# Performance work log

Hardware: AMD Instinct MI355X
Metric: run time of the kernel (lower is better)

## Reference

```python
import jax, jax.numpy as jnp
import numpy as np

B, F, R, C = 16384, 256, 32, 16
H1, H2 = 128, 32        # FS-MLP hidden sizes
G1, G2 = 256, 64        # consequent MLP hidden sizes


def setup_inputs() -> dict:
    key = jax.random.key(0)
    ks = jax.random.split(key, 16)
    s = 0.05
    return {
        "data": jax.random.normal(ks[0], (B, F), jnp.float32),
        # per-rule antecedent params (torch inits proto=0, var=1; randomize proto for a nontrivial test)
        "proto": jax.random.normal(ks[1], (R, F), jnp.float32) * 0.1,
        "var": jnp.full((R, F), 0.05, jnp.float32),
        # shared FS-MLP: Linear(F,128)->ReLU->Linear(128,32)->ReLU->Linear(32,1)->ReLU
        "Wf1": jax.random.normal(ks[2], (H1, F), jnp.float32) * s,
        "bf1": jax.random.normal(ks[3], (H1,), jnp.float32) * s,
        "Wf2": jax.random.normal(ks[4], (H2, H1), jnp.float32) * s,
        "bf2": jax.random.normal(ks[5], (H2,), jnp.float32) * s,
        "Wf3": jax.random.normal(ks[6], (1, H2), jnp.float32) * s,
        "bf3": jax.random.normal(ks[7], (1,), jnp.float32) * s,
        # per-rule consequent MLP (stacked over rule dim): Linear(F,256)->ELU->Linear(256,64)->ELU->Linear(64,C)
        "Wc1": jax.random.normal(ks[8], (R, G1, F), jnp.float32) * s,
        "bc1": jax.random.normal(ks[9], (R, G1), jnp.float32) * s,
        "Wc2": jax.random.normal(ks[10], (R, G2, G1), jnp.float32) * s,
        "bc2": jax.random.normal(ks[11], (R, G2), jnp.float32) * s,
        "Wc3": jax.random.normal(ks[12], (R, C, G2), jnp.float32) * s,
        "bc3": jax.random.normal(ks[13], (R, C), jnp.float32) * s,
    }


def reference(data, proto, var, Wf1, bf1, Wf2, bf2, Wf3, bf3,
              Wc1, bc1, Wc2, bc2, Wc3, bc3):
    # Antecedent: Gaussian membership per rule -> [R, B, F]
    v = jnp.clip(var, 1e-4, 0.1)
    mem = jnp.exp(-(data[None, :, :] - proto[:, None, :]) ** 2
                  / (2.0 * v[:, None, :] ** 2))
    # Shared firing-strength MLP on each rule's membership tensor -> [R, B]
    h = jax.nn.relu(jnp.einsum('rbf,of->rbo', mem, Wf1) + bf1)
    h = jax.nn.relu(jnp.einsum('rbo,po->rbp', h, Wf2) + bf2)
    fs_ini = jax.nn.relu(jnp.einsum('rbp,qp->rbq', h, Wf3) + bf3)[..., 0]
    fire_strength = jax.nn.softmax(fs_ini.T, axis=1)  # [B, R], softmax over rules
    # Per-rule consequent MLPs on raw data (batched over rule dim) -> [R, B, C]
    c = jax.nn.elu(jnp.einsum('bf,rhf->rbh', data, Wc1) + bc1[:, None, :])
    c = jax.nn.elu(jnp.einsum('rbh,rgh->rbg', c, Wc2) + bc2[:, None, :])
    c = jax.nn.relu(jnp.einsum('rbg,rcg->rbc', c, Wc3) + bc3[:, None, :])
    # Softmax-weighted sum over rules -> [B, C]
    outputs = jnp.einsum('rbc,br->bc', c, fire_strength)
    return outputs, fire_strength
```

## Files before the change

kernel.cpp:

```cpp
#include <hip/hip_runtime.h>
#include <hip/hip_bf16.h>

#define BN 16384
#define FN 256
#define RN 32
#define CN 16
#define H1N 128
#define H2N 32
#define G1N 256
#define G2N 64

typedef __bf16 bf16_t;
typedef __bf16 bf16x8 __attribute__((ext_vector_type(8)));
typedef __bf16 bf16x4 __attribute__((ext_vector_type(4)));
typedef float f32x4 __attribute__((ext_vector_type(4)));

#define OFF_DATA   0UL
#define OFF_WF1    8388608UL
#define OFF_WF2    8454144UL
#define OFF_WC1    8462336UL
#define OFF_WC2    12656640UL
#define OFF_WC3    13705216UL
#define OFF_FSINI  13770752UL
#define OFF_C3     15867904UL

__device__ __forceinline__ f32x4 mfma16(bf16x8 a, bf16x8 b, f32x4 c) {
  return __builtin_amdgcn_mfma_f32_16x16x32_bf16(a, b, c, 0, 0, 0);
}

__device__ __forceinline__ float elu_f(float v) {
  float e = __builtin_amdgcn_exp2f(v * 1.44269504f) - 1.0f;
  return v > 0.f ? v : e;
}

__device__ __forceinline__ bf16x8 lfrag(const char* base, int strideB, int n0, int k0, int lane) {
  int row = n0 + (lane & 15);
  int off = (k0 * 2 + ((lane >> 4) << 4)) ^ ((row & 7) << 4);
  return *(const bf16x8*)(base + row * strideB + off);
}

__device__ __forceinline__ void pack_frag8(const float* __restrict__ src, bf16_t* __restrict__ dst,
                                           int NT, int KS, int g) {
  int per = NT * KS * 64;
  int r = g / per;
  int local = g - r * per;
  int lane = local & 63;
  int fr = local >> 6;
  int ks = fr / NT;
  int nt = fr - ks * NT;
  int N = NT * 16, K = KS * 32;
  int n = nt * 16 + (lane & 15);
  int k = ks * 32 + ((lane >> 4) << 3);
  const float* s = src + (long)r * N * K + (long)n * K + k;
  float4 a = *(const float4*)s;
  float4 b = *(const float4*)(s + 4);
  bf16x8 o;
  o[0] = (bf16_t)a.x; o[1] = (bf16_t)a.y; o[2] = (bf16_t)a.z; o[3] = (bf16_t)a.w;
  o[4] = (bf16_t)b.x; o[5] = (bf16_t)b.y; o[6] = (bf16_t)b.z; o[7] = (bf16_t)b.w;
  *(bf16x8*)(dst + (long)g * 8) = o;
}

#define G_DATA 524288
#define G_WC1  262144
#define G_WC2  65536
#define G_WF1  4096
#define G_WC3  4096
#define G_WF2  512
#define G_TOTAL (G_DATA + G_WC1 + G_WC2 + G_WF1 + G_WC3 + G_WF2)

__global__ __launch_bounds__(256) void k0_pack(
    const float* __restrict__ data, const float* __restrict__ Wf1, const float* __restrict__ Wf2,
    const float* __restrict__ Wc1, const float* __restrict__ Wc2, const float* __restrict__ Wc3,
    char* __restrict__ ws)
{
  int g = blockIdx.x * 256 + threadIdx.x;
  if (g < G_DATA) {
    const float* s = data + (long)g * 8;
    float4 a = *(const float4*)s, b = *(const float4*)(s + 4);
    bf16x8 o;
    o[0] = (bf16_t)a.x; o[1] = (bf16_t)a.y; o[2] = (bf16_t)a.z; o[3] = (bf16_t)a.w;
    o[4] = (bf16_t)b.x; o[5] = (bf16_t)b.y; o[6] = (bf16_t)b.z; o[7] = (bf16_t)b.w;
    *(bf16x8*)((bf16_t*)(ws + OFF_DATA) + (long)g * 8) = o;
    return;
  }
  g -= G_DATA;
  if (g < G_WC1) { pack_frag8(Wc1, (bf16_t*)(ws + OFF_WC1), 16, 8, g); return; }
  g -= G_WC1;
  if (g < G_WC2) { pack_frag8(Wc2, (bf16_t*)(ws + OFF_WC2), 4, 8, g); return; }
  g -= G_WC2;
  if (g < G_WF1) { pack_frag8(Wf1, (bf16_t*)(ws + OFF_WF1), 8, 8, g); return; }
  g -= G_WF1;
  if (g < G_WC3) { pack_frag8(Wc3, (bf16_t*)(ws + OFF_WC3), 1, 2, g); return; }
  g -= G_WC3;
  if (g < G_WF2) { pack_frag8(Wf2, (bf16_t*)(ws + OFF_WF2), 2, 4, g); return; }
}

__global__ __launch_bounds__(512) void k1_fs(
    const float* __restrict__ data, const float* __restrict__ proto, const float* __restrict__ var,
    const float* __restrict__ bf1g, const float* __restrict__ bf2g,
    const float* __restrict__ Wf3g, const float* __restrict__ bf3g,
    const bf16_t* __restrict__ Wf1p, const bf16_t* __restrict__ Wf2p,
    float* __restrict__ fsini)
{
  __shared__ float proto_s[FN];
  __shared__ float ivar_s[FN];
  __shared__ __attribute__((aligned(16))) char fs_lds[36864];

  const int r   = blockIdx.x >> 8;
  const int b0  = (blockIdx.x & 255) << 6;
  const int tid = threadIdx.x;
  const int lane = tid & 63;
  const int w   = tid >> 6;

  if (tid < FN) {
    proto_s[tid] = proto[r * FN + tid];
    float v = var[r * FN + tid];
    v = fminf(fmaxf(v, 1e-4f), 0.1f);
    ivar_s[tid] = 1.4426950408889634f * 0.5f / (v * v);
  }
  __syncthreads();

  {
    const int row = tid >> 3;
    const int f0  = (tid & 7) << 5;
    const float* dp = data + (long)(b0 + row) * FN + f0;
    char* mrow = fs_lds + row * 512;
    const int sw = (row & 7) << 4;
    #pragma unroll
    for (int i = 0; i < 4; ++i) {
      const int f = f0 + i * 8;
      float4 x0 = *(const float4*)(dp + i * 8);
      float4 x1 = *(const float4*)(dp + i * 8 + 4);
      bf16x8 m; float d;
      d = x0.x - proto_s[f + 0]; m[0] = (bf16_t)__builtin_amdgcn_exp2f(-d * d * ivar_s[f + 0]);
      d = x0.y - proto_s[f + 1]; m[1] = (bf16_t)__builtin_amdgcn_exp2f(-d * d * ivar_s[f + 1]);
      d = x0.z - proto_s[f + 2]; m[2] = (bf16_t)__builtin_amdgcn_exp2f(-d * d * ivar_s[f + 2]);
      d = x0.w - proto_s[f + 3]; m[3] = (bf16_t)__builtin_amdgcn_exp2f(-d * d * ivar_s[f + 3]);
      d = x1.x - proto_s[f + 4]; m[4] = (bf16_t)__builtin_amdgcn_exp2f(-d * d * ivar_s[f + 4]);
      d = x1.y - proto_s[f + 5]; m[5] = (bf16_t)__builtin_amdgcn_exp2f(-d * d * ivar_s[f + 5]);
      d = x1.z - proto_s[f + 6]; m[6] = (bf16_t)__builtin_amdgcn_exp2f(-d * d * ivar_s[f + 6]);
      d = x1.w - proto_s[f + 7]; m[7] = (bf16_t)__builtin_amdgcn_exp2f(-d * d * ivar_s[f + 7]);
      *(bf16x8*)(mrow + ((f * 2) ^ sw)) = m;
    }
  }
  __syncthreads();

  const int mg = w >> 1;
  const int ng = w & 1;
  f32x4 acc[2][2] = {};
  #pragma unroll
  for (int ks = 0; ks < 8; ++ks) {
    bf16x8 a[2], bb[2];
    #pragma unroll
    for (int i = 0; i < 2; ++i)
      a[i] = *(const bf16x8*)(Wf1p + (((ks * 8 + mg * 2 + i) * 64 + lane)) * 8);
    #pragma unroll
    for (int j = 0; j < 2; ++j)
      bb[j] = lfrag(fs_lds, 512, (ng * 2 + j) * 16, ks * 32, lane);
    #pragma unroll
    for (int i = 0; i < 2; ++i)
      #pragma unroll
      for (int j = 0; j < 2; ++j)
        acc[i][j] = mfma16(a[i], bb[j], acc[i][j]);
  }
  __syncthreads();

  #pragma unroll
  for (int i = 0; i < 2; ++i) {
    const int hb = (mg * 2 + i) * 16 + ((lane >> 4) << 2);
    f32x4 bias = *(const f32x4*)(bf1g + hb);
    #pragma unroll
    for (int j = 0; j < 2; ++j) {
      const int b = (ng * 2 + j) * 16 + (lane & 15);
      bf16x4 o;
      #pragma unroll
      for (int q = 0; q < 4; ++q)
        o[q] = (bf16_t)fmaxf(acc[i][j][q] + bias[q], 0.f);
      *(bf16x4*)(fs_lds + b * 256 + ((hb * 2) ^ ((b & 7) << 4))) = o;
    }
  }
  __syncthreads();

  bf16_t* h2t = (bf16_t*)(fs_lds + 32768);
  {
    const int m = w >> 2;
    const int n = w & 3;
    f32x4 acc2 = {};
    #pragma unroll
    for (int ks = 0; ks < 4; ++ks) {
      bf16x8 a = *(const bf16x8*)(Wf2p + (((ks * 2 + m) * 64 + lane)) * 8);
      bf16x8 bb = lfrag(fs_lds, 256, n * 16, ks * 32, lane);
      acc2 = mfma16(a, bb, acc2);
    }
    const int p0 = m * 16 + ((lane >> 4) << 2);
    const int b  = n * 16 + (lane & 15);
    f32x4 bias = *(const f32x4*)(bf2g + p0);
    #pragma unroll
    for (int q = 0; q < 4; ++q)
      h2t[(p0 + q) * 64 + b] = (bf16_t)fmaxf(acc2[q] + bias[q], 0.f);
  }
  __syncthreads();

  if (tid < 64) {
    float s = bf3g[0];
    #pragma unroll
    for (int p = 0; p < H2N; ++p) s += (float)h2t[p * 64 + tid] * Wf3g[p];
    fsini[(long)(b0 + tid) * RN + r] = fmaxf(s, 0.f);
  }
}

__global__ __launch_bounds__(256) void k2_softmax(const float* __restrict__ fsini,
                                                  float* __restrict__ fire)
{
  int b = blockIdx.x * 256 + threadIdx.x;
  float v[RN];
  const float4* p = (const float4*)(fsini + (long)b * RN);
  #pragma unroll
  for (int i = 0; i < RN / 4; ++i) {
    float4 t = p[i];
    v[4 * i] = t.x; v[4 * i + 1] = t.y; v[4 * i + 2] = t.z; v[4 * i + 3] = t.w;
  }
  float m = v[0];
  #pragma unroll
  for (int i = 1; i < RN; ++i) m = fmaxf(m, v[i]);
  float s = 0.f;
  #pragma unroll
  for (int i = 0; i < RN; ++i) { v[i] = expf(v[i] - m); s += v[i]; }
  float inv = 1.f / s;
  float4* o = (float4*)(fire + (long)b * RN);
  #pragma unroll
  for (int i = 0; i < RN / 4; ++i) {
    float4 t; t.x = v[4 * i] * inv; t.y = v[4 * i + 1] * inv;
    t.z = v[4 * i + 2] * inv; t.w = v[4 * i + 3] * inv;
    o[i] = t;
  }
}

__global__ __launch_bounds__(512) void k3_cons(
    const bf16_t* __restrict__ datab,
    const bf16_t* __restrict__ Wc1p, const bf16_t* __restrict__ Wc2p, const bf16_t* __restrict__ Wc3p,
    const float* __restrict__ bc1, const float* __restrict__ bc2, const float* __restrict__ bc3,
    float* __restrict__ c3buf)
{
  __shared__ __attribute__((aligned(16))) char a_lds[64 * 512];
  __shared__ __attribute__((aligned(16))) char c2_lds[64 * 128];

  const int bid = blockIdx.x;
  const int xcd = bid & 7;
  const int kk  = bid >> 3;
  const int r   = xcd * 4 + (kk >> 8);
  const int b0  = (kk & 255) << 6;

  const int tid = threadIdx.x;
  const int lane = tid & 63;
  const int w   = tid >> 6;

  {
    const int row = tid >> 3;
    const int e0  = (tid & 7) << 5;
    const bf16_t* sp = datab + (long)(b0 + row) * FN + e0;
    char* drow = a_lds + row * 512;
    const int sw = (row & 7) << 4;
    #pragma unroll
    for (int i = 0; i < 4; ++i) {
      bf16x8 v = *(const bf16x8*)(sp + i * 8);
      *(bf16x8*)(drow + (((e0 + i * 8) * 2) ^ sw)) = v;
    }
  }
  __syncthreads();

  const int wm = w >> 1;
  const int wn = w & 1;
  const bf16_t* W1 = Wc1p + (long)r * G1N * FN;
  f32x4 acc[4][2] = {};
  #pragma unroll
  for (int ks = 0; ks < 8; ++ks) {
    bf16x8 a[4], bb[2];
    #pragma unroll
    for (int i = 0; i < 4; ++i)
      a[i] = *(const bf16x8*)(W1 + (((ks * 16 + wm * 4 + i) * 64 + lane)) * 8);
    #pragma unroll
    for (int j = 0; j < 2; ++j)
      bb[j] = lfrag(a_lds, 512, (wn * 2 + j) * 16, ks * 32, lane);
    #pragma unroll
    for (int i = 0; i < 4; ++i)
      #pragma unroll
      for (int j = 0; j < 2; ++j)
        acc[i][j] = mfma16(a[i], bb[j], acc[i][j]);
  }
  __syncthreads();

  #pragma unroll
  for (int i = 0; i < 4; ++i) {
    const int g1b = (wm * 4 + i) * 16 + ((lane >> 4) << 2);
    f32x4 bias = *(const f32x4*)(bc1 + r * G1N + g1b);
    #pragma unroll
    for (int j = 0; j < 2; ++j) {
      const int b = (wn * 2 + j) * 16 + (lane & 15);
      bf16x4 o;
      #pragma unroll
      for (int q = 0; q < 4; ++q)
        o[q] = (bf16_t)elu_f(acc[i][j][q] + bias[q]);
      *(bf16x4*)(a_lds + b * 512 + ((g1b * 2) ^ ((b & 7) << 4))) = o;
    }
  }
  __syncthreads();

  const int m2 = w >> 1;
  const int n2 = w & 1;
  const bf16_t* W2 = Wc2p + (long)r * G2N * G1N;
  f32x4 acc2[2] = {};
  #pragma unroll
  for (int ks = 0; ks < 8; ++ks) {
    bf16x8 a = *(const bf16x8*)(W2 + (((ks * 4 + m2) * 64 + lane)) * 8);
    #pragma unroll
    for (int j = 0; j < 2; ++j) {
      bf16x8 bb = lfrag(a_lds, 512, (n2 * 2 + j) * 16, ks * 32, lane);
      acc2[j] = mfma16(a, bb, acc2[j]);
    }
  }
  {
    const int g2b = m2 * 16 + ((lane >> 4) << 2);
    f32x4 bias = *(const f32x4*)(bc2 + r * G2N + g2b);
    #pragma unroll
    for (int j = 0; j < 2; ++j) {
      const int b = (n2 * 2 + j) * 16 + (lane & 15);
      bf16x4 o;
      #pragma unroll
      for (int q = 0; q < 4; ++q)
        o[q] = (bf16_t)elu_f(acc2[j][q] + bias[q]);
      *(bf16x4*)(c2_lds + b * 128 + ((g2b * 2) ^ ((b & 7) << 4))) = o;
    }
  }
  __syncthreads();

  if (w < 4) {
    const bf16_t* W3 = Wc3p + (long)r * CN * G2N;
    f32x4 acc3 = {};
    #pragma unroll
    for (int ks = 0; ks < 2; ++ks) {
      bf16x8 a = *(const bf16x8*)(W3 + (((long)ks * 64 + lane)) * 8);
      bf16x8 bb = lfrag(c2_lds, 128, w * 16, ks * 32, lane);
      acc3 = mfma16(a, bb, acc3);
    }
    const int c0 = ((lane >> 4) << 2);
    const int b  = w * 16 + (lane & 15);
    f32x4 bias = *(const f32x4*)(bc3 + r * CN + c0);
    f32x4 o;
    #pragma unroll
    for (int q = 0; q < 4; ++q) o[q] = fmaxf(acc3[q] + bias[q], 0.f);
    *(f32x4*)(c3buf + ((long)r * BN + b0 + b) * CN + c0) = o;
  }
}

__global__ __launch_bounds__(256) void k4_out(const float* __restrict__ c3buf,
                                              const float* __restrict__ fire,
                                              float* __restrict__ out)
{
  int t = blockIdx.x * 256 + threadIdx.x;
  int b = t >> 2, c4 = (t & 3) << 2;
  const float* fp = fire + (long)b * RN;
  f32x4 s = {};
  #pragma unroll
  for (int rr = 0; rr < RN; ++rr) {
    float fw = fp[rr];
    f32x4 v = *(const f32x4*)(c3buf + ((long)rr * BN + b) * CN + c4);
    s += fw * v;
  }
  *(f32x4*)(out + (long)b * CN + c4) = s;
}

extern "C" void kernel_launch(void* const* d_in, const int* in_sizes, int n_in,
                              void* d_out, int out_size, void* d_ws, size_t ws_size,
                              hipStream_t stream) {
  const float* data = (const float*)d_in[0];
  const float* proto = (const float*)d_in[1];
  const float* var  = (const float*)d_in[2];
  const float* Wf1  = (const float*)d_in[3];
  const float* bf1  = (const float*)d_in[4];
  const float* Wf2  = (const float*)d_in[5];
  const float* bf2  = (const float*)d_in[6];
  const float* Wf3  = (const float*)d_in[7];
  const float* bf3  = (const float*)d_in[8];
  const float* Wc1  = (const float*)d_in[9];
  const float* bc1  = (const float*)d_in[10];
  const float* Wc2  = (const float*)d_in[11];
  const float* bc2  = (const float*)d_in[12];
  const float* Wc3  = (const float*)d_in[13];
  const float* bc3  = (const float*)d_in[14];

  char* ws = (char*)d_ws;
  bf16_t* datab = (bf16_t*)(ws + OFF_DATA);
  bf16_t* Wf1p  = (bf16_t*)(ws + OFF_WF1);
  bf16_t* Wf2p  = (bf16_t*)(ws + OFF_WF2);
  bf16_t* Wc1p  = (bf16_t*)(ws + OFF_WC1);
  bf16_t* Wc2p  = (bf16_t*)(ws + OFF_WC2);
  bf16_t* Wc3p  = (bf16_t*)(ws + OFF_WC3);
  float*  fsini = (float*)(ws + OFF_FSINI);
  float*  c3buf = (float*)(ws + OFF_C3);

  float* out  = (float*)d_out;
  float* fire = out + (long)BN * CN;

  k0_pack<<<G_TOTAL / 256, 256, 0, stream>>>(data, Wf1, Wf2, Wc1, Wc2, Wc3, ws);
  k1_fs<<<RN * (BN / 64), 512, 0, stream>>>(data, proto, var, bf1, bf2, Wf3, bf3,
                                            Wf1p, Wf2p, fsini);
  k2_softmax<<<BN / 256, 256, 0, stream>>>(fsini, fire);
  k3_cons<<<RN * (BN / 64), 512, 0, stream>>>(datab, Wc1p, Wc2p, Wc3p, bc1, bc2, bc3, c3buf);
  k4_out<<<(BN * CN / 4) / 256, 256, 0, stream>>>(c3buf, fire, out);
}
```

Baseline: 255.1 us.

## Process four rules per block in firing-strength kernel and raise MFMA wave priority

The firing-strength kernel now handles four rules per block. Each block loads its data tile into registers once and loops over the rules, which cuts the grid from 32×256 to 8×256 blocks and reuses each data row four times instead of re-reading it from global memory. In exchange the kernel holds more registers, runs serial per-rule phases with extra barriers, and has fewer blocks available to hide latency. Separately, the consequent kernel raises wave priority with s_setprio around its MFMA loops so matrix work gets issued ahead of other waves.

```diff
diff --git a/kernel.cpp b/kernel.cpp
--- a/kernel.cpp
+++ b/kernel.cpp
@@ -102,110 +102,127 @@
     const bf16_t* __restrict__ Wf1p, const bf16_t* __restrict__ Wf2p,
     float* __restrict__ fsini)
 {
-  __shared__ float proto_s[FN];
-  __shared__ float ivar_s[FN];
+  __shared__ float proto_s[4][FN];
+  __shared__ float ivar_s[4][FN];
   __shared__ __attribute__((aligned(16))) char fs_lds[36864];
 
-  const int r   = blockIdx.x >> 8;
-  const int b0  = (blockIdx.x & 255) << 6;
+  const int bid = blockIdx.x;
+  const int rg  = bid >> 8;
+  const int b0  = (bid & 255) << 6;
   const int tid = threadIdx.x;
   const int lane = tid & 63;
   const int w   = tid >> 6;
 
-  if (tid < FN) {
-    proto_s[tid] = proto[r * FN + tid];
-    float v = var[r * FN + tid];
+  #pragma unroll
+  for (int k = 0; k < 2; ++k) {
+    int idx = tid + k * 512;
+    int rr = idx >> 8, f = idx & 255;
+    int r = rg * 4 + rr;
+    proto_s[rr][f] = proto[r * FN + f];
+    float v = var[r * FN + f];
     v = fminf(fmaxf(v, 1e-4f), 0.1f);
-    ivar_s[tid] = 1.4426950408889634f * 0.5f / (v * v);
+    ivar_s[rr][f] = 1.4426950408889634f * 0.5f / (v * v);
+  }
+
+  const int row = tid >> 3;
+  const int f0  = (tid & 7) << 5;
+  float4 dreg[8];
+  {
+    const float* dp = data + (long)(b0 + row) * FN + f0;
+    #pragma unroll
+    for (int i = 0; i < 8; ++i) dreg[i] = *(const float4*)(dp + i * 4);
   }
   __syncthreads();
 
-  {
-    const int row = tid >> 3;
-    const int f0  = (tid & 7) << 5;
-    const float* dp = data + (long)(b0 + row) * FN + f0;
-    char* mrow = fs_lds + row * 512;
-    const int sw = (row & 7) << 4;
-    #pragma unroll
-    for (int i = 0; i < 4; ++i) {
-      const int f = f0 + i * 8;
-      float4 x0 = *(const float4*)(dp + i * 8);
-      float4 x1 = *(const float4*)(dp + i * 8 + 4);
-      bf16x8 m; float d;
-      d = x0.x - proto_s[f + 0]; m[0] = (bf16_t)__builtin_amdgcn_exp2f(-d * d * ivar_s[f + 0]);
-      d = x0.y - proto_s[f + 1]; m[1] = (bf16_t)__builtin_amdgcn_exp2f(-d * d * ivar_s[f + 1]);
-      d = x0.z - proto_s[f + 2]; m[2] = (bf16_t)__builtin_amdgcn_exp2f(-d * d * ivar_s[f + 2]);
-      d = x0.w - proto_s[f + 3]; m[3] = (bf16_t)__builtin_amdgcn_exp2f(-d * d * ivar_s[f + 3]);
-      d = x1.x - proto_s[f + 4]; m[4] = (bf16_t)__builtin_amdgcn_exp2f(-d * d * ivar_s[f + 4]);
-      d = x1.y - proto_s[f + 5]; m[5] = (bf16_t)__builtin_amdgcn_exp2f(-d * d * ivar_s[f + 5]);
-      d = x1.z - proto_s[f + 6]; m[6] = (bf16_t)__builtin_amdgcn_exp2f(-d * d * ivar_s[f + 6]);
-      d = x1.w - proto_s[f + 7]; m[7] = (bf16_t)__builtin_amdgcn_exp2f(-d * d * ivar_s[f + 7]);
-      *(bf16x8*)(mrow + ((f * 2) ^ sw)) = m;
-    }
-  }
-  __syncthreads();
-
-  const int mg = w >> 1;
-  const int ng = w & 1;
-  f32x4 acc[2][2] = {};
-  #pragma unroll
-  for (int ks = 0; ks < 8; ++ks) {
-    bf16x8 a[2], bb[2];
-    #pragma unroll
-    for (int i = 0; i < 2; ++i)
-      a[i] = *(const bf16x8*)(Wf1p + (((ks * 8 + mg * 2 + i) * 64 + lane)) * 8);
-    #pragma unroll
-    for (int j = 0; j < 2; ++j)
-      bb[j] = lfrag(fs_lds, 512, (ng * 2 + j) * 16, ks * 32, lane);
-    #pragma unroll
-    for (int i = 0; i < 2; ++i)
+  bf16_t* h2t = (bf16_t*)(fs_lds + 32768);
+  char* mrow = fs_lds + row * 512;
+  const int sw = (row & 7) << 4;
+
+  for (int rr = 0; rr < 4; ++rr) {
+    const int r = rg * 4 + rr;
+
+    {
+      #pragma unroll
+      for (int i = 0; i < 4; ++i) {
+        const int f = f0 + i * 8;
+        float4 x0 = dreg[i * 2];
+        float4 x1 = dreg[i * 2 + 1];
+        bf16x8 m; float d;
+        d = x0.x - proto_s[rr][f + 0]; m[0] = (bf16_t)__builtin_amdgcn_exp2f(-d * d * ivar_s[rr][f + 0]);
+        d = x0.y - proto_s[rr][f + 1]; m[1] = (bf16_t)__builtin_amdgcn_exp2f(-d * d * ivar_s[rr][f + 1]);
+        d = x0.z - proto_s[rr][f + 2]; m[2] = (bf16_t)__builtin_amdgcn_exp2f(-d * d * ivar_s[rr][f + 2]);
+        d = x0.w - proto_s[rr][f + 3]; m[3] = (bf16_t)__builtin_amdgcn_exp2f(-d * d * ivar_s[rr][f + 3]);
+        d = x1.x - proto_s[rr][f + 4]; m[4] = (bf16_t)__builtin_amdgcn_exp2f(-d * d * ivar_s[rr][f + 4]);
+        d = x1.y - proto_s[rr][f + 5]; m[5] = (bf16_t)__builtin_amdgcn_exp2f(-d * d * ivar_s[rr][f + 5]);
+        d = x1.z - proto_s[rr][f + 6]; m[6] = (bf16_t)__builtin_amdgcn_exp2f(-d * d * ivar_s[rr][f + 6]);
+        d = x1.w - proto_s[rr][f + 7]; m[7] = (bf16_t)__builtin_amdgcn_exp2f(-d * d * ivar_s[rr][f + 7]);
+        *(bf16x8*)(mrow + ((f * 2) ^ sw)) = m;
+      }
+    }
+    __syncthreads();
+
+    const int mg = w >> 1;
+    const int ng = w & 1;
+    f32x4 acc[2][2] = {};
+    #pragma unroll
+    for (int ks = 0; ks < 8; ++ks) {
+      bf16x8 a[2], bb[2];
+      #pragma unroll
+      for (int i = 0; i < 2; ++i)
+        a[i] = *(const bf16x8*)(Wf1p + (((ks * 8 + mg * 2 + i) * 64 + lane)) * 8);
       #pragma unroll
       for (int j = 0; j < 2; ++j)
-        acc[i][j] = mfma16(a[i], bb[j], acc[i][j]);
-  }
-  __syncthreads();
-
-  #pragma unroll
-  for (int i = 0; i < 2; ++i) {
-    const int hb = (mg * 2 + i) * 16 + ((lane >> 4) << 2);
-    f32x4 bias = *(const f32x4*)(bf1g + hb);
-    #pragma unroll
-    for (int j = 0; j < 2; ++j) {
-      const int b = (ng * 2 + j) * 16 + (lane & 15);
-      bf16x4 o;
+        bb[j] = lfrag(fs_lds, 512, (ng * 2 + j) * 16, ks * 32, lane);
+      #pragma unroll
+      for (int i = 0; i < 2; ++i)
+        #pragma unroll
+        for (int j = 0; j < 2; ++j)
+          acc[i][j] = mfma16(a[i], bb[j], acc[i][j]);
+    }
+    __syncthreads();
+
+    #pragma unroll
+    for (int i = 0; i < 2; ++i) {
+      const int hb = (mg * 2 + i) * 16 + ((lane >> 4) << 2);
+      f32x4 bias = *(const f32x4*)(bf1g + hb);
+      #pragma unroll
+      for (int j = 0; j < 2; ++j) {
+        const int b = (ng * 2 + j) * 16 + (lane & 15);
+        bf16x4 o;
+        #pragma unroll
+        for (int q = 0; q < 4; ++q)
+          o[q] = (bf16_t)fmaxf(acc[i][j][q] + bias[q], 0.f);
+        *(bf16x4*)(fs_lds + b * 256 + ((hb * 2) ^ ((b & 7) << 4))) = o;
+      }
+    }
+    __syncthreads();
+
+    {
+      const int m = w >> 2;
+      const int n = w & 3;
+      f32x4 acc2 = {};
+      #pragma unroll
+      for (int ks = 0; ks < 4; ++ks) {
+        bf16x8 a = *(const bf16x8*)(Wf2p + (((ks * 2 + m) * 64 + lane)) * 8);
+        bf16x8 bb = lfrag(fs_lds, 256, n * 16, ks * 32, lane);
+        acc2 = mfma16(a, bb, acc2);
+      }
+      const int p0 = m * 16 + ((lane >> 4) << 2);
+      const int b  = n * 16 + (lane & 15);
+      f32x4 bias = *(const f32x4*)(bf2g + p0);
       #pragma unroll
       for (int q = 0; q < 4; ++q)
-        o[q] = (bf16_t)fmaxf(acc[i][j][q] + bias[q], 0.f);
-      *(bf16x4*)(fs_lds + b * 256 + ((hb * 2) ^ ((b & 7) << 4))) = o;
-    }
-  }
-  __syncthreads();
-
-  bf16_t* h2t = (bf16_t*)(fs_lds + 32768);
-  {
-    const int m = w >> 2;
-    const int n = w & 3;
-    f32x4 acc2 = {};
-    #pragma unroll
-    for (int ks = 0; ks < 4; ++ks) {
-      bf16x8 a = *(const bf16x8*)(Wf2p + (((ks * 2 + m) * 64 + lane)) * 8);
-      bf16x8 bb = lfrag(fs_lds, 256, n * 16, ks * 32, lane);
-      acc2 = mfma16(a, bb, acc2);
-    }
-    const int p0 = m * 16 + ((lane >> 4) << 2);
-    const int b  = n * 16 + (lane & 15);
-    f32x4 bias = *(const f32x4*)(bf2g + p0);
-    #pragma unroll
-    for (int q = 0; q < 4; ++q)
-      h2t[(p0 + q) * 64 + b] = (bf16_t)fmaxf(acc2[q] + bias[q], 0.f);
-  }
-  __syncthreads();
-
-  if (tid < 64) {
-    float s = bf3g[0];
-    #pragma unroll
-    for (int p = 0; p < H2N; ++p) s += (float)h2t[p * 64 + tid] * Wf3g[p];
-    fsini[(long)(b0 + tid) * RN + r] = fmaxf(s, 0.f);
+        h2t[(p0 + q) * 64 + b] = (bf16_t)fmaxf(acc2[q] + bias[q], 0.f);
+    }
+    __syncthreads();
+
+    if (tid < 64) {
+      float s = bf3g[0];
+      #pragma unroll
+      for (int p = 0; p < H2N; ++p) s += (float)h2t[p * 64 + tid] * Wf3g[p];
+      fsini[(long)(b0 + tid) * RN + r] = fmaxf(s, 0.f);
+    }
+    __syncthreads();
   }
 }
 
@@ -273,6 +290,7 @@
   const int wn = w & 1;
   const bf16_t* W1 = Wc1p + (long)r * G1N * FN;
   f32x4 acc[4][2] = {};
+  __builtin_amdgcn_s_setprio(1);
   #pragma unroll
   for (int ks = 0; ks < 8; ++ks) {
     bf16x8 a[4], bb[2];
@@ -288,6 +306,7 @@
       for (int j = 0; j < 2; ++j)
         acc[i][j] = mfma16(a[i], bb[j], acc[i][j]);
   }
+  __builtin_amdgcn_s_setprio(0);
   __syncthreads();
 
   #pragma unroll
@@ -310,6 +329,7 @@
   const int n2 = w & 1;
   const bf16_t* W2 = Wc2p + (long)r * G2N * G1N;
   f32x4 acc2[2] = {};
+  __builtin_amdgcn_s_setprio(1);
   #pragma unroll
   for (int ks = 0; ks < 8; ++ks) {
     bf16x8 a = *(const bf16x8*)(W2 + (((ks * 4 + m2) * 64 + lane)) * 8);
@@ -319,6 +339,7 @@
       acc2[j] = mfma16(a, bb, acc2[j]);
     }
   }
+  __builtin_amdgcn_s_setprio(0);
   {
     const int g2b = m2 * 16 + ((lane >> 4) << 2);
     f32x4 bias = *(const f32x4*)(bc2 + r * G2N + g2b);
@@ -403,8 +424,8 @@
   float* fire = out + (long)BN * CN;
 
   k0_pack<<<G_TOTAL / 256, 256, 0, stream>>>(data, Wf1, Wf2, Wc1, Wc2, Wc3, ws);
-  k1_fs<<<RN * (BN / 64), 512, 0, stream>>>(data, proto, var, bf1, bf2, Wf3, bf3,
-                                            Wf1p, Wf2p, fsini);
+  k1_fs<<<8 * (BN / 64), 512, 0, stream>>>(data, proto, var, bf1, bf2, Wf3, bf3,
+                                           Wf1p, Wf2p, fsini);
   k2_softmax<<<BN / 256, 256, 0, stream>>>(fsini, fire);
   k3_cons<<<RN * (BN / 64), 512, 0, stream>>>(datab, Wc1p, Wc2p, Wc3p, bc1, bc2, bc3, c3buf);
   k4_out<<<(BN * CN / 4) / 256, 256, 0, stream>>>(c3buf, fire, out);
```

Result: slower. 262.2 us (+2.8%).

## Merge firing-strength and consequent kernels into one interleaved launch

Applied to the files above, without the earlier changes.

The firing-strength kernel and the consequent MLP kernel become device functions called from a single kernel. Odd blocks run the firing-strength path and even blocks the consequent path, with one shared LDS buffer sized for the larger of the two. This removes a launch and the serialization between two independent stages, so memory-heavy and MFMA-heavy blocks can run at the same time on the CUs. The risks are that register pressure is now set by the heavier body for both paths, and the consequent kernel's XCD-aware rule mapping is disturbed because its block ids are now halved.

```diff
diff --git a/kernel.cpp b/kernel.cpp
--- a/kernel.cpp
+++ b/kernel.cpp
@@ -95,19 +95,21 @@
   if (g < G_WF2) { pack_frag8(Wf2, (bf16_t*)(ws + OFF_WF2), 2, 4, g); return; }
 }
 
-__global__ __launch_bounds__(512) void k1_fs(
+__device__ __forceinline__ void k1_body(
+    char* smem, int bid,
     const float* __restrict__ data, const float* __restrict__ proto, const float* __restrict__ var,
     const float* __restrict__ bf1g, const float* __restrict__ bf2g,
     const float* __restrict__ Wf3g, const float* __restrict__ bf3g,
     const bf16_t* __restrict__ Wf1p, const bf16_t* __restrict__ Wf2p,
     float* __restrict__ fsini)
 {
-  __shared__ float proto_s[FN];
-  __shared__ float ivar_s[FN];
-  __shared__ __attribute__((aligned(16))) char fs_lds[36864];
-
-  const int r   = blockIdx.x >> 8;
-  const int b0  = (blockIdx.x & 255) << 6;
+  char* fs_lds   = smem;
+  bf16_t* h2t    = (bf16_t*)(smem + 32768);
+  float* proto_s = (float*)(smem + 36864);
+  float* ivar_s  = (float*)(smem + 37888);
+
+  const int r   = bid >> 8;
+  const int b0  = (bid & 255) << 6;
   const int tid = threadIdx.x;
   const int lane = tid & 63;
   const int w   = tid >> 6;
@@ -181,7 +183,6 @@
   }
   __syncthreads();
 
-  bf16_t* h2t = (bf16_t*)(fs_lds + 32768);
   {
     const int m = w >> 2;
     const int n = w & 3;
@@ -209,43 +210,16 @@
   }
 }
 
-__global__ __launch_bounds__(256) void k2_softmax(const float* __restrict__ fsini,
-                                                  float* __restrict__ fire)
-{
-  int b = blockIdx.x * 256 + threadIdx.x;
-  float v[RN];
-  const float4* p = (const float4*)(fsini + (long)b * RN);
-  #pragma unroll
-  for (int i = 0; i < RN / 4; ++i) {
-    float4 t = p[i];
-    v[4 * i] = t.x; v[4 * i + 1] = t.y; v[4 * i + 2] = t.z; v[4 * i + 3] = t.w;
-  }
-  float m = v[0];
-  #pragma unroll
-  for (int i = 1; i < RN; ++i) m = fmaxf(m, v[i]);
-  float s = 0.f;
-  #pragma unroll
-  for (int i = 0; i < RN; ++i) { v[i] = expf(v[i] - m); s += v[i]; }
-  float inv = 1.f / s;
-  float4* o = (float4*)(fire + (long)b * RN);
-  #pragma unroll
-  for (int i = 0; i < RN / 4; ++i) {
-    float4 t; t.x = v[4 * i] * inv; t.y = v[4 * i + 1] * inv;
-    t.z = v[4 * i + 2] * inv; t.w = v[4 * i + 3] * inv;
-    o[i] = t;
-  }
-}
-
-__global__ __launch_bounds__(512) void k3_cons(
+__device__ __forceinline__ void k3_body(
+    char* smem, int bid,
     const bf16_t* __restrict__ datab,
     const bf16_t* __restrict__ Wc1p, const bf16_t* __restrict__ Wc2p, const bf16_t* __restrict__ Wc3p,
     const float* __restrict__ bc1, const float* __restrict__ bc2, const float* __restrict__ bc3,
     float* __restrict__ c3buf)
 {
-  __shared__ __attribute__((aligned(16))) char a_lds[64 * 512];
-  __shared__ __attribute__((aligned(16))) char c2_lds[64 * 128];
-
-  const int bid = blockIdx.x;
+  char* a_lds  = smem;
+  char* c2_lds = smem + 32768;
+
   const int xcd = bid & 7;
   const int kk  = bid >> 3;
   const int r   = xcd * 4 + (kk >> 8);
@@ -350,6 +324,53 @@
     #pragma unroll
     for (int q = 0; q < 4; ++q) o[q] = fmaxf(acc3[q] + bias[q], 0.f);
     *(f32x4*)(c3buf + ((long)r * BN + b0 + b) * CN + c0) = o;
+  }
+}
+
+__global__ __launch_bounds__(512) void k13_fused(
+    const float* __restrict__ data, const float* __restrict__ proto, const float* __restrict__ var,
+    const float* __restrict__ bf1g, const float* __restrict__ bf2g,
+    const float* __restrict__ Wf3g, const float* __restrict__ bf3g,
+    const bf16_t* __restrict__ Wf1p, const bf16_t* __restrict__ Wf2p,
+    float* __restrict__ fsini,
+    const bf16_t* __restrict__ datab,
+    const bf16_t* __restrict__ Wc1p, const bf16_t* __restrict__ Wc2p, const bf16_t* __restrict__ Wc3p,
+    const float* __restrict__ bc1, const float* __restrict__ bc2, const float* __restrict__ bc3,
+    float* __restrict__ c3buf)
+{
+  __shared__ __attribute__((aligned(16))) char smem[40960];
+  const int bid = blockIdx.x;
+  if (bid & 1) {
+    k1_body(smem, bid >> 1, data, proto, var, bf1g, bf2g, Wf3g, bf3g, Wf1p, Wf2p, fsini);
+  } else {
+    k3_body(smem, bid >> 1, datab, Wc1p, Wc2p, Wc3p, bc1, bc2, bc3, c3buf);
+  }
+}
+
+__global__ __launch_bounds__(256) void k2_softmax(const float* __restrict__ fsini,
+                                                  float* __restrict__ fire)
+{
+  int b = blockIdx.x * 256 + threadIdx.x;
+  float v[RN];
+  const float4* p = (const float4*)(fsini + (long)b * RN);
+  #pragma unroll
+  for (int i = 0; i < RN / 4; ++i) {
+    float4 t = p[i];
+    v[4 * i] = t.x; v[4 * i + 1] = t.y; v[4 * i + 2] = t.z; v[4 * i + 3] = t.w;
+  }
+  float m = v[0];
+  #pragma unroll
+  for (int i = 1; i < RN; ++i) m = fmaxf(m, v[i]);
+  float s = 0.f;
+  #pragma unroll
+  for (int i = 0; i < RN; ++i) { v[i] = expf(v[i] - m); s += v[i]; }
+  float inv = 1.f / s;
+  float4* o = (float4*)(fire + (long)b * RN);
+  #pragma unroll
+  for (int i = 0; i < RN / 4; ++i) {
+    float4 t; t.x = v[4 * i] * inv; t.y = v[4 * i + 1] * inv;
+    t.z = v[4 * i + 2] * inv; t.w = v[4 * i + 3] * inv;
+    o[i] = t;
   }
 }
 
@@ -403,9 +424,9 @@
   float* fire = out + (long)BN * CN;
 
   k0_pack<<<G_TOTAL / 256, 256, 0, stream>>>(data, Wf1, Wf2, Wc1, Wc2, Wc3, ws);
-  k1_fs<<<RN * (BN / 64), 512, 0, stream>>>(data, proto, var, bf1, bf2, Wf3, bf3,
-                                            Wf1p, Wf2p, fsini);
+  k13_fused<<<2 * RN * (BN / 64), 512, 0, stream>>>(
+      data, proto, var, bf1, bf2, Wf3, bf3, Wf1p, Wf2p, fsini,
+      datab, Wc1p, Wc2p, Wc3p, bc1, bc2, bc3, c3buf);
   k2_softmax<<<BN / 256, 256, 0, stream>>>(fsini, fire);
-  k3_cons<<<RN * (BN / 64), 512, 0, stream>>>(datab, Wc1p, Wc2p, Wc3p, bc1, bc2, bc3, c3buf);
   k4_out<<<(BN * CN / 4) / 256, 256, 0, stream>>>(c3buf, fire, out);
 }
```

Measured after the change: 253.2 us. Within noise of the previous version (-0.8%).

## Fuse firing-strength, softmax, consequent MLPs and rule reduction into one kernel

Applied to the files above, without the earlier changes.

Replaces the four kernels (FS-MLP, softmax, consequent MLPs, weighted sum) with a single kernel where each block owns 32 batch rows and loops over all 32 rules. Firing strengths and the softmax stay in shared memory, and the weighted reduction is accumulated in registers, so the fsini and per-rule c3 intermediates no longer go through global memory. In exchange the tile shrinks to 32 rows, giving lower MFMA reuse per weight load, and every block rereads all rule weights. The grid also drops to 512 blocks, each of which runs a long serial rule loop with many barriers.

```diff
diff --git a/kernel.cpp b/kernel.cpp
--- a/kernel.cpp
+++ b/kernel.cpp
@@ -21,8 +21,13 @@
 #define OFF_WC1    8462336UL
 #define OFF_WC2    12656640UL
 #define OFF_WC3    13705216UL
-#define OFF_FSINI  13770752UL
-#define OFF_C3     15867904UL
+
+#define L_FIRE  0
+#define L_PV    4352
+#define L_DATA  6400
+#define L_C1    22784
+#define L_C2    39168
+#define L_TOT   43264
 
 __device__ __forceinline__ f32x4 mfma16(bf16x8 a, bf16x8 b, f32x4 c) {
   return __builtin_amdgcn_mfma_f32_16x16x32_bf16(a, b, c, 0, 0, 0);
@@ -95,279 +100,242 @@
   if (g < G_WF2) { pack_frag8(Wf2, (bf16_t*)(ws + OFF_WF2), 2, 4, g); return; }
 }
 
-__global__ __launch_bounds__(512) void k1_fs(
+__global__ __launch_bounds__(512) void k_mega(
     const float* __restrict__ data, const float* __restrict__ proto, const float* __restrict__ var,
     const float* __restrict__ bf1g, const float* __restrict__ bf2g,
     const float* __restrict__ Wf3g, const float* __restrict__ bf3g,
     const bf16_t* __restrict__ Wf1p, const bf16_t* __restrict__ Wf2p,
-    float* __restrict__ fsini)
+    const bf16_t* __restrict__ datab,
+    const bf16_t* __restrict__ Wc1p, const bf16_t* __restrict__ Wc2p, const bf16_t* __restrict__ Wc3p,
+    const float* __restrict__ bc1, const float* __restrict__ bc2, const float* __restrict__ bc3,
+    float* __restrict__ out, float* __restrict__ fire_g)
 {
-  __shared__ float proto_s[FN];
-  __shared__ float ivar_s[FN];
-  __shared__ __attribute__((aligned(16))) char fs_lds[36864];
-
-  const int r   = blockIdx.x >> 8;
-  const int b0  = (blockIdx.x & 255) << 6;
+  __shared__ __attribute__((aligned(16))) char smem[L_TOT];
+  float* fire_s  = (float*)(smem + L_FIRE);
+  float* proto_s = (float*)(smem + L_PV);
+  float* ivar_s  = (float*)(smem + L_PV + 1024);
+  char*  dmem    = smem + L_DATA;
+  char*  c1r     = smem + L_C1;
+  bf16_t* h2t    = (bf16_t*)(smem + L_C2);
+  char*  c2r     = smem + L_C2;
+
+  const int bid = blockIdx.x;
+  const int b0  = bid << 5;
   const int tid = threadIdx.x;
   const int lane = tid & 63;
   const int w   = tid >> 6;
 
-  if (tid < FN) {
-    proto_s[tid] = proto[r * FN + tid];
-    float v = var[r * FN + tid];
-    v = fminf(fmaxf(v, 1e-4f), 0.1f);
-    ivar_s[tid] = 1.4426950408889634f * 0.5f / (v * v);
+  const int arow = tid >> 4;
+  const int af0  = (tid & 15) << 4;
+  float4 dreg[4];
+  {
+    const float* dp = data + (long)(b0 + arow) * FN + af0;
+    #pragma unroll
+    for (int i = 0; i < 4; ++i) dreg[i] = *(const float4*)(dp + i * 4);
+  }
+
+  for (int r = 0; r < RN; ++r) {
+    __syncthreads();
+    if (tid < FN) {
+      proto_s[tid] = proto[r * FN + tid];
+      float v = var[r * FN + tid];
+      v = fminf(fmaxf(v, 1e-4f), 0.1f);
+      ivar_s[tid] = 1.4426950408889634f * 0.5f / (v * v);
+    }
+    __syncthreads();
+
+    {
+      char* mrow = dmem + arow * 512;
+      const int sw = (arow & 7) << 4;
+      #pragma unroll
+      for (int i = 0; i < 2; ++i) {
+        const int f = af0 + i * 8;
+        float4 x0 = dreg[i * 2];
+        float4 x1 = dreg[i * 2 + 1];
+        bf16x8 m; float d;
+        d = x0.x - proto_s[f + 0]; m[0] = (bf16_t)__builtin_amdgcn_exp2f(-d * d * ivar_s[f + 0]);
+        d = x0.y - proto_s[f + 1]; m[1] = (bf16_t)__builtin_amdgcn_exp2f(-d * d * ivar_s[f + 1]);
+        d = x0.z - proto_s[f + 2]; m[2] = (bf16_t)__builtin_amdgcn_exp2f(-d * d * ivar_s[f + 2]);
+        d = x0.w - proto_s[f + 3]; m[3] = (bf16_t)__builtin_amdgcn_exp2f(-d * d * ivar_s[f + 3]);
+        d = x1.x - proto_s[f + 4]; m[4] = (bf16_t)__builtin_amdgcn_exp2f(-d * d * ivar_s[f + 4]);
+        d = x1.y - proto_s[f + 5]; m[5] = (bf16_t)__builtin_amdgcn_exp2f(-d * d * ivar_s[f + 5]);
+        d = x1.z - proto_s[f + 6]; m[6] = (bf16_t)__builtin_amdgcn_exp2f(-d * d * ivar_s[f + 6]);
+        d = x1.w - proto_s[f + 7]; m[7] = (bf16_t)__builtin_amdgcn_exp2f(-d * d * ivar_s[f + 7]);
+        *(bf16x8*)(mrow + ((f * 2) ^ sw)) = m;
+      }
+    }
+    __syncthreads();
+
+    f32x4 acc[2] = {};
+    #pragma unroll
+    for (int ks = 0; ks < 8; ++ks) {
+      bf16x8 a = *(const bf16x8*)(Wf1p + (((ks * 8 + w) * 64 + lane)) * 8);
+      #pragma unroll
+      for (int j = 0; j < 2; ++j) {
+        bf16x8 bb = lfrag(dmem, 512, j * 16, ks * 32, lane);
+        acc[j] = mfma16(a, bb, acc[j]);
+      }
+    }
+    {
+      const int hb = w * 16 + ((lane >> 4) << 2);
+      f32x4 bias = *(const f32x4*)(bf1g + hb);
+      #pragma unroll
+      for (int j = 0; j < 2; ++j) {
+        const int b = j * 16 + (lane & 15);
+        bf16x4 o;
+        #pragma unroll
+        for (int q = 0; q < 4; ++q)
+          o[q] = (bf16_t)fmaxf(acc[j][q] + bias[q], 0.f);
+        *(bf16x4*)(c1r + b * 256 + ((hb * 2) ^ ((b & 7) << 4))) = o;
+      }
+    }
+    __syncthreads();
+
+    if (w < 4) {
+      const int m = w >> 1;
+      const int n = w & 1;
+      f32x4 acc2 = {};
+      #pragma unroll
+      for (int ks = 0; ks < 4; ++ks) {
+        bf16x8 a = *(const bf16x8*)(Wf2p + (((ks * 2 + m) * 64 + lane)) * 8);
+        bf16x8 bb = lfrag(c1r, 256, n * 16, ks * 32, lane);
+        acc2 = mfma16(a, bb, acc2);
+      }
+      const int p0 = m * 16 + ((lane >> 4) << 2);
+      const int b  = n * 16 + (lane & 15);
+      f32x4 bias = *(const f32x4*)(bf2g + p0);
+      #pragma unroll
+      for (int q = 0; q < 4; ++q)
+        h2t[(p0 + q) * 32 + b] = (bf16_t)fmaxf(acc2[q] + bias[q], 0.f);
+    }
+    __syncthreads();
+
+    if (tid < 32) {
+      float s = bf3g[0];
+      #pragma unroll
+      for (int p = 0; p < H2N; ++p) s += (float)h2t[p * 32 + tid] * Wf3g[p];
+      fire_s[tid * 33 + r] = fmaxf(s, 0.f);
+    }
   }
   __syncthreads();
 
+  if (tid < 32) {
+    float* row = fire_s + tid * 33;
+    float m = row[0];
+    #pragma unroll
+    for (int i = 1; i < RN; ++i) m = fmaxf(m, row[i]);
+    float s = 0.f;
+    float e[RN];
+    #pragma unroll
+    for (int i = 0; i < RN; ++i) { e[i] = expf(row[i] - m); s += e[i]; }
+    float inv = 1.f / s;
+    #pragma unroll
+    for (int i = 0; i < RN; ++i) row[i] = e[i] * inv;
+  }
+  __syncthreads();
+
   {
-    const int row = tid >> 3;
-    const int f0  = (tid & 7) << 5;
-    const float* dp = data + (long)(b0 + row) * FN + f0;
-    char* mrow = fs_lds + row * 512;
+    int idx = tid;
+    #pragma unroll
+    for (int t = 0; t < 2; ++t) {
+      int rr = idx >> 5, ii = idx & 31;
+      fire_g[(long)(b0 + rr) * RN + ii] = fire_s[rr * 33 + ii];
+      idx += 512;
+    }
+    const int row = tid >> 4;
+    const int e0  = (tid & 15) << 4;
+    const bf16_t* sp = datab + (long)(b0 + row) * FN + e0;
+    char* drow = dmem + row * 512;
     const int sw = (row & 7) << 4;
     #pragma unroll
-    for (int i = 0; i < 4; ++i) {
-      const int f = f0 + i * 8;
-      float4 x0 = *(const float4*)(dp + i * 8);
-      float4 x1 = *(const float4*)(dp + i * 8 + 4);
-      bf16x8 m; float d;
-      d = x0.x - proto_s[f + 0]; m[0] = (bf16_t)__builtin_amdgcn_exp2f(-d * d * ivar_s[f + 0]);
-      d = x0.y - proto_s[f + 1]; m[1] = (bf16_t)__builtin_amdgcn_exp2f(-d * d * ivar_s[f + 1]);
-      d = x0.z - proto_s[f + 2]; m[2] = (bf16_t)__builtin_amdgcn_exp2f(-d * d * ivar_s[f + 2]);
-      d = x0.w - proto_s[f + 3]; m[3] = (bf16_t)__builtin_amdgcn_exp2f(-d * d * ivar_s[f + 3]);
-      d = x1.x - proto_s[f + 4]; m[4] = (bf16_t)__builtin_amdgcn_exp2f(-d * d * ivar_s[f + 4]);
-      d = x1.y - proto_s[f + 5]; m[5] = (bf16_t)__builtin_amdgcn_exp2f(-d * d * ivar_s[f + 5]);
-      d = x1.z - proto_s[f + 6]; m[6] = (bf16_t)__builtin_amdgcn_exp2f(-d * d * ivar_s[f + 6]);
-      d = x1.w - proto_s[f + 7]; m[7] = (bf16_t)__builtin_amdgcn_exp2f(-d * d * ivar_s[f + 7]);
-      *(bf16x8*)(mrow + ((f * 2) ^ sw)) = m;
-    }
-  }
-  __syncthreads();
-
-  const int mg = w >> 1;
-  const int ng = w & 1;
-  f32x4 acc[2][2] = {};
-  #pragma unroll
-  for (int ks = 0; ks < 8; ++ks) {
-    bf16x8 a[2], bb[2];
-    #pragma unroll
-    for (int i = 0; i < 2; ++i)
-      a[i] = *(const bf16x8*)(Wf1p + (((ks * 8 + mg * 2 + i) * 64 + lane)) * 8);
-    #pragma unroll
-    for (int j = 0; j < 2; ++j)
-      bb[j] = lfrag(fs_lds, 512, (ng * 2 + j) * 16, ks * 32, lane);
-    #pragma unroll
-    for (int i = 0; i < 2; ++i)
-      #pragma unroll
-      for (int j = 0; j < 2; ++j)
-        acc[i][j] = mfma16(a[i], bb[j], acc[i][j]);
-  }
-  __syncthreads();
-
-  #pragma unroll
-  for (int i = 0; i < 2; ++i) {
-    const int hb = (mg * 2 + i) * 16 + ((lane >> 4) << 2);
-    f32x4 bias = *(const f32x4*)(bf1g + hb);
-    #pragma unroll
-    for (int j = 0; j < 2; ++j) {
-      const int b = (ng * 2 + j) * 16 + (lane & 15);
-      bf16x4 o;
-      #pragma unroll
-      for (int q = 0; q < 4; ++q)
-        o[q] = (bf16_t)fmaxf(acc[i][j][q] + bias[q], 0.f);
-      *(bf16x4*)(fs_lds + b * 256 + ((hb * 2) ^ ((b & 7) << 4))) = o;
-    }
-  }
-  __syncthreads();
-
-  bf16_t* h2t = (bf16_t*)(fs_lds + 32768);
-  {
-    const int m = w >> 2;
-    const int n = w & 3;
-    f32x4 acc2 = {};
-    #pragma unroll
-    for (int ks = 0; ks < 4; ++ks) {
-      bf16x8 a = *(const bf16x8*)(Wf2p + (((ks * 2 + m) * 64 + lane)) * 8);
-      bf16x8 bb = lfrag(fs_lds, 256, n * 16, ks * 32, lane);
-      acc2 = mfma16(a, bb, acc2);
-    }
-    const int p0 = m * 16 + ((lane >> 4) << 2);
-    const int b  = n * 16 + (lane & 15);
-    f32x4 bias = *(const f32x4*)(bf2g + p0);
-    #pragma unroll
-    for (int q = 0; q < 4; ++q)
-      h2t[(p0 + q) * 64 + b] = (bf16_t)fmaxf(acc2[q] + bias[q], 0.f);
-  }
-  __syncthreads();
-
-  if (tid < 64) {
-    float s = bf3g[0];
-    #pragma unroll
-    for (int p = 0; p < H2N; ++p) s += (float)h2t[p * 64 + tid] * Wf3g[p];
-    fsini[(long)(b0 + tid) * RN + r] = fmaxf(s, 0.f);
-  }
-}
-
-__global__ __launch_bounds__(256) void k2_softmax(const float* __restrict__ fsini,
-                                                  float* __restrict__ fire)
-{
-  int b = blockIdx.x * 256 + threadIdx.x;
-  float v[RN];
-  const float4* p = (const float4*)(fsini + (long)b * RN);
-  #pragma unroll
-  for (int i = 0; i < RN / 4; ++i) {
-    float4 t = p[i];
-    v[4 * i] = t.x; v[4 * i + 1] = t.y; v[4 * i + 2] = t.z; v[4 * i + 3] = t.w;
-  }
-  float m = v[0];
-  #pragma unroll
-  for (int i = 1; i < RN; ++i) m = fmaxf(m, v[i]);
-  float s = 0.f;
-  #pragma unroll
-  for (int i = 0; i < RN; ++i) { v[i] = expf(v[i] - m); s += v[i]; }
-  float inv = 1.f / s;
-  float4* o = (float4*)(fire + (long)b * RN);
-  #pragma unroll
-  for (int i = 0; i < RN / 4; ++i) {
-    float4 t; t.x = v[4 * i] * inv; t.y = v[4 * i + 1] * inv;
-    t.z = v[4 * i + 2] * inv; t.w = v[4 * i + 3] * inv;
-    o[i] = t;
-  }
-}
-
-__global__ __launch_bounds__(512) void k3_cons(
-    const bf16_t* __restrict__ datab,
-    const bf16_t* __restrict__ Wc1p, const bf16_t* __restrict__ Wc2p, const bf16_t* __restrict__ Wc3p,
-    const float* __restrict__ bc1, const float* __restrict__ bc2, const float* __restrict__ bc3,
-    float* __restrict__ c3buf)
-{
-  __shared__ __attribute__((aligned(16))) char a_lds[64 * 512];
-  __shared__ __attribute__((aligned(16))) char c2_lds[64 * 128];
-
-  const int bid = blockIdx.x;
-  const int xcd = bid & 7;
-  const int kk  = bid >> 3;
-  const int r   = xcd * 4 + (kk >> 8);
-  const int b0  = (kk & 255) << 6;
-
-  const int tid = threadIdx.x;
-  const int lane = tid & 63;
-  const int w   = tid >> 6;
-
-  {
-    const int row = tid >> 3;
-    const int e0  = (tid & 7) << 5;
-    const bf16_t* sp = datab + (long)(b0 + row) * FN + e0;
-    char* drow = a_lds + row * 512;
-    const int sw = (row & 7) << 4;
-    #pragma unroll
-    for (int i = 0; i < 4; ++i) {
+    for (int i = 0; i < 2; ++i) {
       bf16x8 v = *(const bf16x8*)(sp + i * 8);
       *(bf16x8*)(drow + (((e0 + i * 8) * 2) ^ sw)) = v;
     }
   }
   __syncthreads();
 
-  const int wm = w >> 1;
-  const int wn = w & 1;
-  const bf16_t* W1 = Wc1p + (long)r * G1N * FN;
-  f32x4 acc[4][2] = {};
-  #pragma unroll
-  for (int ks = 0; ks < 8; ++ks) {
-    bf16x8 a[4], bb[2];
-    #pragma unroll
-    for (int i = 0; i < 4; ++i)
-      a[i] = *(const bf16x8*)(W1 + (((ks * 16 + wm * 4 + i) * 64 + lane)) * 8);
-    #pragma unroll
-    for (int j = 0; j < 2; ++j)
-      bb[j] = lfrag(a_lds, 512, (wn * 2 + j) * 16, ks * 32, lane);
-    #pragma unroll
-    for (int i = 0; i < 4; ++i)
+  f32x4 acc_out = {};
+  for (int r = 0; r < RN; ++r) {
+    const bf16_t* W1 = Wc1p + (long)r * G1N * FN;
+    f32x4 acc[2][2] = {};
+    #pragma unroll
+    for (int ks = 0; ks < 8; ++ks) {
+      bf16x8 a[2], bb[2];
+      #pragma unroll
+      for (int i = 0; i < 2; ++i)
+        a[i] = *(const bf16x8*)(W1 + (((ks * 16 + w * 2 + i) * 64 + lane)) * 8);
       #pragma unroll
       for (int j = 0; j < 2; ++j)
-        acc[i][j] = mfma16(a[i], bb[j], acc[i][j]);
-  }
-  __syncthreads();
-
-  #pragma unroll
-  for (int i = 0; i < 4; ++i) {
-    const int g1b = (wm * 4 + i) * 16 + ((lane >> 4) << 2);
-    f32x4 bias = *(const f32x4*)(bc1 + r * G1N + g1b);
-    #pragma unroll
-    for (int j = 0; j < 2; ++j) {
-      const int b = (wn * 2 + j) * 16 + (lane & 15);
+        bb[j] = lfrag(dmem, 512, j * 16, ks * 32, lane);
+      #pragma unroll
+      for (int i = 0; i < 2; ++i)
+        #pragma unroll
+        for (int j = 0; j < 2; ++j)
+          acc[i][j] = mfma16(a[i], bb[j], acc[i][j]);
+    }
+    #pragma unroll
+    for (int i = 0; i < 2; ++i) {
+      const int g1b = (w * 2 + i) * 16 + ((lane >> 4) << 2);
+      f32x4 bias = *(const f32x4*)(bc1 + r * G1N + g1b);
+      #pragma unroll
+      for (int j = 0; j < 2; ++j) {
+        const int b = j * 16 + (lane & 15);
+        bf16x4 o;
+        #pragma unroll
+        for (int q = 0; q < 4; ++q)
+          o[q] = (bf16_t)elu_f(acc[i][j][q] + bias[q]);
+        *(bf16x4*)(c1r + b * 512 + ((g1b * 2) ^ ((b & 7) << 4))) = o;
+      }
+    }
+    __syncthreads();
+
+    {
+      const int m2 = w >> 1;
+      const int n2 = w & 1;
+      const bf16_t* W2 = Wc2p + (long)r * G2N * G1N;
+      f32x4 acc2 = {};
+      #pragma unroll
+      for (int ks = 0; ks < 8; ++ks) {
+        bf16x8 a = *(const bf16x8*)(W2 + (((ks * 4 + m2) * 64 + lane)) * 8);
+        bf16x8 bb = lfrag(c1r, 512, n2 * 16, ks * 32, lane);
+        acc2 = mfma16(a, bb, acc2);
+      }
+      const int g2b = m2 * 16 + ((lane >> 4) << 2);
+      const int b = n2 * 16 + (lane & 15);
+      f32x4 bias = *(const f32x4*)(bc2 + r * G2N + g2b);
       bf16x4 o;
       #pragma unroll
       for (int q = 0; q < 4; ++q)
-        o[q] = (bf16_t)elu_f(acc[i][j][q] + bias[q]);
-      *(bf16x4*)(a_lds + b * 512 + ((g1b * 2) ^ ((b & 7) << 4))) = o;
-    }
-  }
-  __syncthreads();
-
-  const int m2 = w >> 1;
-  const int n2 = w & 1;
-  const bf16_t* W2 = Wc2p + (long)r * G2N * G1N;
-  f32x4 acc2[2] = {};
-  #pragma unroll
-  for (int ks = 0; ks < 8; ++ks) {
-    bf16x8 a = *(const bf16x8*)(W2 + (((ks * 4 + m2) * 64 + lane)) * 8);
-    #pragma unroll
-    for (int j = 0; j < 2; ++j) {
-      bf16x8 bb = lfrag(a_lds, 512, (n2 * 2 + j) * 16, ks * 32, lane);
-      acc2[j] = mfma16(a, bb, acc2[j]);
-    }
-  }
-  {
-    const int g2b = m2 * 16 + ((lane >> 4) << 2);
-    f32x4 bias = *(const f32x4*)(bc2 + r * G2N + g2b);
-    #pragma unroll
-    for (int j = 0; j < 2; ++j) {
-      const int b = (n2 * 2 + j) * 16 + (lane & 15);
-      bf16x4 o;
+        o[q] = (bf16_t)elu_f(acc2[q] + bias[q]);
+      *(bf16x4*)(c2r + b * 128 + ((g2b * 2) ^ ((b & 7) << 4))) = o;
+    }
+    __syncthreads();
+
+    if (w < 2) {
+      const bf16_t* W3 = Wc3p + (long)r * CN * G2N;
+      f32x4 acc3 = {};
+      #pragma unroll
+      for (int ks = 0; ks < 2; ++ks) {
+        bf16x8 a = *(const bf16x8*)(W3 + (((long)ks * 64 + lane)) * 8);
+        bf16x8 bb = lfrag(c2r, 128, w * 16, ks * 32, lane);
+        acc3 = mfma16(a, bb, acc3);
+      }
+      const int c0 = ((lane >> 4) << 2);
+      const int b  = w * 16 + (lane & 15);
+      const float fw = fire_s[b * 33 + r];
+      f32x4 bias = *(const f32x4*)(bc3 + r * CN + c0);
       #pragma unroll
       for (int q = 0; q < 4; ++q)
-        o[q] = (bf16_t)elu_f(acc2[j][q] + bias[q]);
-      *(bf16x4*)(c2_lds + b * 128 + ((g2b * 2) ^ ((b & 7) << 4))) = o;
-    }
-  }
-  __syncthreads();
-
-  if (w < 4) {
-    const bf16_t* W3 = Wc3p + (long)r * CN * G2N;
-    f32x4 acc3 = {};
-    #pragma unroll
-    for (int ks = 0; ks < 2; ++ks) {
-      bf16x8 a = *(const bf16x8*)(W3 + (((long)ks * 64 + lane)) * 8);
-      bf16x8 bb = lfrag(c2_lds, 128, w * 16, ks * 32, lane);
-      acc3 = mfma16(a, bb, acc3);
-    }
+        acc_out[q] += fw * fmaxf(acc3[q] + bias[q], 0.f);
+    }
+  }
+
+  if (w < 2) {
     const int c0 = ((lane >> 4) << 2);
     const int b  = w * 16 + (lane & 15);
-    f32x4 bias = *(const f32x4*)(bc3 + r * CN + c0);
-    f32x4 o;
-    #pragma unroll
-    for (int q = 0; q < 4; ++q) o[q] = fmaxf(acc3[q] + bias[q], 0.f);
-    *(f32x4*)(c3buf + ((long)r * BN + b0 + b) * CN + c0) = o;
-  }
-}
-
-__global__ __launch_bounds__(256) void k4_out(const float* __restrict__ c3buf,
-                                              const float* __restrict__ fire,
-                                              float* __restrict__ out)
-{
-  int t = blockIdx.x * 256 + threadIdx.x;
-  int b = t >> 2, c4 = (t & 3) << 2;
-  const float* fp = fire + (long)b * RN;
-  f32x4 s = {};
-  #pragma unroll
-  for (int rr = 0; rr < RN; ++rr) {
-    float fw = fp[rr];
-    f32x4 v = *(const f32x4*)(c3buf + ((long)rr * BN + b) * CN + c4);
-    s += fw * v;
-  }
-  *(f32x4*)(out + (long)b * CN + c4) = s;
+    *(f32x4*)(out + (long)(b0 + b) * CN + c0) = acc_out;
+  }
 }
 
 extern "C" void kernel_launch(void* const* d_in, const int* in_sizes, int n_in,
@@ -396,16 +364,12 @@
   bf16_t* Wc1p  = (bf16_t*)(ws + OFF_WC1);
   bf16_t* Wc2p  = (bf16_t*)(ws + OFF_WC2);
   bf16_t* Wc3p  = (bf16_t*)(ws + OFF_WC3);
-  float*  fsini = (float*)(ws + OFF_FSINI);
-  float*  c3buf = (float*)(ws + OFF_C3);
 
   float* out  = (float*)d_out;
   float* fire = out + (long)BN * CN;
 
   k0_pack<<<G_TOTAL / 256, 256, 0, stream>>>(data, Wf1, Wf2, Wc1, Wc2, Wc3, ws);
-  k1_fs<<<RN * (BN / 64), 512, 0, stream>>>(data, proto, var, bf1, bf2, Wf3, bf3,
-                                            Wf1p, Wf2p, fsini);
-  k2_softmax<<<BN / 256, 256, 0, stream>>>(fsini, fire);
-  k3_cons<<<RN * (BN / 64), 512, 0, stream>>>(datab, Wc1p, Wc2p, Wc3p, bc1, bc2, bc3, c3buf);
-  k4_out<<<(BN * CN / 4) / 256, 256, 0, stream>>>(c3buf, fire, out);
-}
+  k_mega<<<BN / 32, 512, 0, stream>>>(
+      data, proto, var, bf1, bf2, Wf3, bf3, Wf1p, Wf2p,
+      datab, Wc1p, Wc2p, Wc3p, bc1, bc2, bc3, out, fire);
+}
```

Result: slower. 403.1 us (+58.0%).
